# Kernel optimization log

Measured on AMD Instinct MI355X. Metric: run time of the kernel, lower is better.

## Reference

```python
import jax, jax.numpy as jnp
import numpy as np

PC_RANGE = (-54.0, -54.0, -5.0, 54.0, 54.0, 3.0)
VOXEL = (0.075, 0.075, 0.2)
STRIDE = 8
FW = 180  # feature map size along x
FH = 180  # feature map size along y
NUM_CLASS = 2
M = 500   # num_max_objs
MIN_RADIUS = 2
OVERLAP = 0.1
C_IN = 128
HM_C = 2
REG_C = 9
B = 4


def conv2d(x, w, b=None):
    y = jax.lax.conv_general_dilated(x, w, (1, 1), 'SAME',
                                     dimension_numbers=('NCHW', 'OIHW', 'NCHW'))
    return y if b is None else y + b[None, :, None, None]


def bn(x, g, b, m, v, eps=1e-5):
    inv = g / jnp.sqrt(v + eps)
    return x * inv[None, :, None, None] + (b - m * inv)[None, :, None, None]


def gaussian_radius(height, width, min_overlap):
    # centernet_utils.gaussian_radius
    b1 = height + width
    c1 = width * height * (1.0 - min_overlap) / (1.0 + min_overlap)
    r1 = (b1 + jnp.sqrt(jnp.maximum(b1 * b1 - 4.0 * c1, 0.0))) / 2.0
    b2 = 2.0 * (height + width)
    c2 = (1.0 - min_overlap) * width * height
    r2 = (b2 + jnp.sqrt(jnp.maximum(b2 * b2 - 16.0 * c2, 0.0))) / 2.0
    a3 = 4.0 * min_overlap
    b3 = -2.0 * min_overlap * (height + width)
    c3 = (min_overlap - 1.0) * width * height
    r3 = (b3 + jnp.sqrt(jnp.maximum(b3 * b3 - 4.0 * a3 * c3, 0.0))) / (2.0 * a3)
    return jnp.minimum(jnp.minimum(r1, r2), r3)


def assign_targets(gt):
    # gt: (B, M, 8) = [x, y, z, dx, dy, dz, ry, cls]; cls==0 / zero box = padding
    x, y, z = gt[..., 0], gt[..., 1], gt[..., 2]
    dx, dy, dz, ry = gt[..., 3], gt[..., 4], gt[..., 5], gt[..., 6]
    cls = gt[..., 7].astype(jnp.int32)
    coord_x = jnp.clip((x - PC_RANGE[0]) / VOXEL[0] / STRIDE, 0.0, FW - 0.5)
    coord_y = jnp.clip((y - PC_RANGE[1]) / VOXEL[1] / STRIDE, 0.0, FH - 0.5)
    cxi = coord_x.astype(jnp.int32)
    cyi = coord_y.astype(jnp.int32)
    dxp = dx / VOXEL[0] / STRIDE
    dyp = dy / VOXEL[1] / STRIDE
    radius = jnp.maximum(gaussian_radius(dxp, dyp, OVERLAP).astype(jnp.int32), MIN_RADIUS)
    valid = (dxp > 0) & (dyp > 0)
    pos = valid & (cls >= 1)

    # --- dense gaussian splat, max-reduced per class (= draw_gaussian_to_heatmap) ---
    ddx = jnp.arange(FW)[None, None, :] - cxi[..., None]   # (B,M,FW)
    ddy = jnp.arange(FH)[None, None, :] - cyi[..., None]   # (B,M,FH)
    sigma = (2.0 * radius.astype(jnp.float32) + 1.0) / 6.0
    d2 = (ddy[..., :, None] ** 2 + ddx[..., None, :] ** 2).astype(jnp.float32)  # (B,M,FH,FW)
    g = jnp.exp(-d2 / (2.0 * sigma[..., None, None] ** 2))
    win = (jnp.abs(ddy) <= radius[..., None])[..., :, None] & \
          (jnp.abs(ddx) <= radius[..., None])[..., None, :]
    g = jnp.where(win & pos[..., None, None], g, 0.0)
    seg = jnp.where(pos, cls - 1, NUM_CLASS)
    hmv = jax.vmap(lambda gv, sv: jax.ops.segment_max(gv, sv, num_segments=NUM_CLASS + 1))(
        g.reshape(B, M, FH * FW), seg)
    heatmap = jnp.maximum(hmv[:, :NUM_CLASS].reshape(B, NUM_CLASS, FH, FW), 0.0)
    heatmap_mask = (heatmap > 0).astype(gt.dtype)

    # --- inds / mask / ret_boxes (5 slots per object: center + 4 neighbors) ---
    base_ind = cyi * FW + cxi
    w_cond = VOXEL[0] * STRIDE > dy / 4.0   # faithful: uses temp_w = gt[:,4]
    l_cond = VOXEL[1] * STRIDE > dx / 4.0   # faithful: uses temp_l = gt[:,3]
    left = cxi - 1 >= 0
    right = cxi + 1 < FW
    up = cyi - 1 >= 0
    down = cyi + 1 < FH
    m0 = jnp.where(valid, jnp.where(cls >= 1, 1, -1), 0)
    s1 = valid & ~w_cond & left
    s2 = valid & ~w_cond & right
    s3 = valid & ~l_cond & up
    s4 = valid & ~l_cond & down
    mask = jnp.stack([m0,
                      jnp.where(s1, m0, 0), jnp.where(s2, m0, 0),
                      jnp.where(s3, m0, 0), jnp.where(s4, m0, 0)], -1).reshape(B, 5 * M)
    inds = jnp.stack([jnp.where(valid, base_ind, 0),
                      jnp.where(s1, base_ind - 1, 0), jnp.where(s2, base_ind + 1, 0),
                      jnp.where(s3, base_ind - FW, 0), jnp.where(s4, base_ind + FW, 0)],
                     -1).reshape(B, 5 * M).astype(jnp.int32)
    offx = coord_x - cxi.astype(gt.dtype)
    offy = coord_y - cyi.astype(gt.dtype)
    base = jnp.stack([offx, offy, z,
                      jnp.log(jnp.maximum(dx, 1e-8)),
                      jnp.log(jnp.maximum(dy, 1e-8)),
                      jnp.log(jnp.maximum(dz, 1e-8)),
                      jnp.cos(ry), jnp.sin(ry)], -1)          # (B,M,8)
    z5 = jnp.zeros((B, M), gt.dtype)
    dx_adj = jnp.stack([z5, s1.astype(gt.dtype), -s2.astype(gt.dtype), z5, z5], -1)  # (B,M,5)
    dy_adj = jnp.stack([z5, z5, z5, s3.astype(gt.dtype), -s4.astype(gt.dtype)], -1)
    zero5 = jnp.zeros_like(dx_adj)
    delta = jnp.stack([dx_adj, dy_adj, zero5, zero5, zero5, zero5, zero5, zero5], -1)  # (B,M,5,8)
    rb = (base[:, :, None, :] + delta) * valid[:, :, None, None].astype(gt.dtype)
    ret_boxes = rb.reshape(B, 5 * M, 8)
    return heatmap, ret_boxes, inds, mask, heatmap_mask


def setup_inputs():
    key = jax.random.key(0)
    ks = jax.random.split(key, 12)
    x = jax.random.normal(ks[0], (B, C_IN, FH, FW), jnp.float32)
    # realistic gt boxes; last 150 per scene are zero padding
    cxy = jax.random.uniform(ks[1], (B, M, 2), minval=-50.0, maxval=50.0)
    zc = jax.random.uniform(ks[2], (B, M, 1), minval=-2.0, maxval=1.0)
    dims = jax.random.uniform(ks[3], (B, M, 3), minval=0.5, maxval=6.0)
    ry = jax.random.uniform(ks[4], (B, M, 1), minval=-3.14, maxval=3.14)
    cls = jax.random.randint(ks[5], (B, M, 1), 1, NUM_CLASS + 1).astype(jnp.float32)
    vm = (jnp.arange(M) < 350)[None, :, None].astype(jnp.float32)
    gt_boxes = jnp.concatenate([cxy, zc, dims, ry, cls], -1) * vm
    p = lambda k, s, sc: jax.random.normal(k, s, jnp.float32) * sc
    return {
        'x': x, 'gt_boxes': gt_boxes,
        'conv1_w': p(ks[6], (C_IN, C_IN, 3, 3), 0.02),
        'bn1_g': jnp.ones((C_IN,)), 'bn1_b': jnp.zeros((C_IN,)),
        'bn1_m': jnp.zeros((C_IN,)), 'bn1_v': jnp.ones((C_IN,)),
        'conv2_w': p(ks[7], (C_IN, C_IN, 3, 3), 0.02),
        'bn2_g': jnp.ones((C_IN,)), 'bn2_b': jnp.zeros((C_IN,)),
        'bn2_m': jnp.zeros((C_IN,)), 'bn2_v': jnp.ones((C_IN,)),
        'hm_w': p(ks[8], (HM_C, C_IN, 3, 3), 0.02),
        'hm_b': jnp.full((HM_C,), -2.19, jnp.float32),
        'reg_w': p(ks[9], (REG_C, C_IN, 3, 3), 0.001),
        'reg_b': jnp.zeros((REG_C,), jnp.float32),
    }


def reference(x, gt_boxes, conv1_w, bn1_g, bn1_b, bn1_m, bn1_v,
              conv2_w, bn2_g, bn2_b, bn2_m, bn2_v, hm_w, hm_b, reg_w, reg_b):
    f = jax.nn.relu(bn(conv2d(x, conv1_w), bn1_g, bn1_b, bn1_m, bn1_v))
    f = jax.nn.relu(bn(conv2d(f, conv2_w), bn2_g, bn2_b, bn2_m, bn2_v))
    hm = conv2d(f, hm_w, hm_b)      # (B, 2, H, W)
    reg = conv2d(f, reg_w, reg_b)   # (B, 9, H, W)
    heatmap, ret_boxes, inds, mask, heatmap_mask = assign_targets(gt_boxes)
    return hm, reg, heatmap, ret_boxes, inds, mask, heatmap_mask
```

## Files before the change

### kernel.cpp

```cpp
#include <hip/hip_runtime.h>
#include <math.h>

typedef unsigned short u16;
typedef short bf16x8 __attribute__((ext_vector_type(8)));
typedef float f32x4 __attribute__((ext_vector_type(4)));

#define FW_ 180
#define FH_ 180
#define HW_ (FW_*FH_)
#define CIN_ 128
#define BB_ 4
#define MM_ 500
#define PW_ 182
#define PADE ((size_t)BB_*PW_*PW_*CIN_)

#define HM_OFF   0
#define REG_OFF  (BB_*2*HW_)
#define HEAT_OFF (REG_OFF + BB_*9*HW_)
#define RB_OFF   (HEAT_OFF + BB_*2*HW_)
#define IND_OFF  (RB_OFF + BB_*MM_*5*8)
#define MSK_OFF  (IND_OFF + BB_*MM_*5)
#define HMM_OFF  (MSK_OFF + BB_*MM_*5)

__device__ inline u16 f2bf(float f) {
    unsigned u = __float_as_uint(f);
    u += 0x7FFFu + ((u >> 16) & 1u);
    return (u16)(u >> 16);
}

#define GLOAD_LDS16(gsrc, ldst) \
    __builtin_amdgcn_global_load_lds( \
        (const __attribute__((address_space(1))) unsigned*)(gsrc), \
        (__attribute__((address_space(3))) unsigned*)(ldst), 16, 0, 0)

__device__ void obj_work(int ob, int lane, const float* __restrict__ gt,
                         float* __restrict__ out)
{
    int b = ob / MM_, m = ob % MM_;
    const float* gp = gt + (size_t)ob * 8;
    float x = gp[0], y = gp[1], z = gp[2];
    float dx = gp[3], dy = gp[4], dz = gp[5], ry = gp[6];
    int cls = (int)gp[7];

    float coord_x = fminf(fmaxf((x + 54.f) / 0.075f / 8.f, 0.f), 179.5f);
    float coord_y = fminf(fmaxf((y + 54.f) / 0.075f / 8.f, 0.f), 179.5f);
    int cxi = (int)coord_x, cyi = (int)coord_y;
    float dxp = dx / 0.075f / 8.f;
    float dyp = dy / 0.075f / 8.f;

    float hgt = dxp, wid = dyp, mo = 0.1f;
    float b1 = hgt + wid, c1 = wid * hgt * (1.f - mo) / (1.f + mo);
    float r1 = (b1 + sqrtf(fmaxf(b1 * b1 - 4.f * c1, 0.f))) * 0.5f;
    float b2 = 2.f * (hgt + wid), c2 = (1.f - mo) * wid * hgt;
    float r2 = (b2 + sqrtf(fmaxf(b2 * b2 - 16.f * c2, 0.f))) * 0.5f;
    float a3 = 4.f * mo, b3 = -2.f * mo * (hgt + wid), c3 = (mo - 1.f) * wid * hgt;
    float r3 = (b3 + sqrtf(fmaxf(b3 * b3 - 4.f * a3 * c3, 0.f))) / (2.f * a3);
    int radius = max((int)fminf(fminf(r1, r2), r3), 2);

    bool valid = (dxp > 0.f) && (dyp > 0.f);
    bool pos = valid && (cls >= 1);

    if (lane == 0) {
        float m0 = valid ? (cls >= 1 ? 1.f : -1.f) : 0.f;
        bool w_cond = (0.075f * 8.f) > dy / 4.f;
        bool l_cond = (0.075f * 8.f) > dx / 4.f;
        bool s1 = valid && !w_cond && (cxi - 1 >= 0);
        bool s2 = valid && !w_cond && (cxi + 1 < FW_);
        bool s3 = valid && !l_cond && (cyi - 1 >= 0);
        bool s4 = valid && !l_cond && (cyi + 1 < FH_);
        int base_ind = cyi * FW_ + cxi;

        float* indp = out + IND_OFF + (size_t)b * MM_ * 5 + m * 5;
        float* mskp = out + MSK_OFF + (size_t)b * MM_ * 5 + m * 5;
        indp[0] = valid ? (float)base_ind : 0.f;
        indp[1] = s1 ? (float)(base_ind - 1) : 0.f;
        indp[2] = s2 ? (float)(base_ind + 1) : 0.f;
        indp[3] = s3 ? (float)(base_ind - FW_) : 0.f;
        indp[4] = s4 ? (float)(base_ind + FW_) : 0.f;
        mskp[0] = m0;
        mskp[1] = s1 ? m0 : 0.f;
        mskp[2] = s2 ? m0 : 0.f;
        mskp[3] = s3 ? m0 : 0.f;
        mskp[4] = s4 ? m0 : 0.f;

        float offx = coord_x - (float)cxi;
        float offy = coord_y - (float)cyi;
        float bse[8] = { offx, offy, z,
                         logf(fmaxf(dx, 1e-8f)), logf(fmaxf(dy, 1e-8f)),
                         logf(fmaxf(dz, 1e-8f)), cosf(ry), sinf(ry) };
        float vm = valid ? 1.f : 0.f;
        float* rbp = out + RB_OFF + ((size_t)b * MM_ + m) * 5 * 8;
#pragma unroll
        for (int s = 0; s < 5; ++s) {
            float t0 = bse[0], t1 = bse[1];
            if (s == 1) t0 += s1 ? 1.f : 0.f;
            if (s == 2) t0 -= s2 ? 1.f : 0.f;
            if (s == 3) t1 += s3 ? 1.f : 0.f;
            if (s == 4) t1 -= s4 ? 1.f : 0.f;
            rbp[s * 8 + 0] = t0 * vm;
            rbp[s * 8 + 1] = t1 * vm;
#pragma unroll
            for (int k = 2; k < 8; ++k) rbp[s * 8 + k] = bse[k] * vm;
        }
    }

    if (pos) {
        float sigma = (2.f * (float)radius + 1.f) / 6.f;
        float inv2s2 = 1.f / (2.f * sigma * sigma);
        int x0 = max(cxi - radius, 0), x1 = min(cxi + radius, FW_ - 1);
        int y0 = max(cyi - radius, 0), y1 = min(cyi + radius, FH_ - 1);
        int wdt = x1 - x0 + 1, tot = wdt * (y1 - y0 + 1);
        float* hp = out + HEAT_OFF + (size_t)(b * 2 + (cls - 1)) * HW_;
        for (int i = lane; i < tot; i += 64) {
            int yy = y0 + i / wdt, xx = x0 + i % wdt;
            float ddy = (float)(yy - cyi), ddx = (float)(xx - cxi);
            float gvl = expf(-(ddy * ddy + ddx * ddx) * inv2s2);
            atomicMax((int*)(hp + yy * FW_ + xx), __float_as_int(gvl));
        }
    }
}

__global__ __launch_bounds__(256) void k_pre(
    const float* __restrict__ x, u16* __restrict__ xT, u16* __restrict__ ws,
    float* __restrict__ out,
    const float* __restrict__ w1, const float* __restrict__ w2,
    const float* __restrict__ hw, const float* __restrict__ rw,
    u16* __restrict__ wT1, u16* __restrict__ wT2, u16* __restrict__ wTh)
{
    __shared__ unsigned lt32[180 * 65];
    int tid = threadIdx.x;
    if (blockIdx.x < 720) {
        int row = blockIdx.x % 180, b = blockIdx.x / 180;
        const float* inr = x + ((size_t)b * CIN_ * FH_ + row) * FW_;
        for (int i = tid; i < 64 * 45; i += 256) {
            int ci2 = i / 45, c4 = i - 45 * ci2;
            const float* p0 = inr + (size_t)(2 * ci2) * HW_ + c4 * 4;
            float4 a = *(const float4*)p0;
            float4 bq = *(const float4*)(p0 + HW_);
            lt32[(c4 * 4 + 0) * 65 + ci2] = (unsigned)f2bf(a.x) | ((unsigned)f2bf(bq.x) << 16);
            lt32[(c4 * 4 + 1) * 65 + ci2] = (unsigned)f2bf(a.y) | ((unsigned)f2bf(bq.y) << 16);
            lt32[(c4 * 4 + 2) * 65 + ci2] = (unsigned)f2bf(a.z) | ((unsigned)f2bf(bq.z) << 16);
            lt32[(c4 * 4 + 3) * 65 + ci2] = (unsigned)f2bf(a.w) | ((unsigned)f2bf(bq.w) << 16);
        }
        __syncthreads();
        unsigned* dst = (unsigned*)(xT + ((size_t)b * PW_ * PW_ + (size_t)(row + 1) * PW_ + 1) * CIN_);
        for (int idx = tid; idx < 180 * 16; idx += 256) {
            int col = idx >> 4, q = idx & 15;
            uint4 v;
            v.x = lt32[col * 65 + q * 4 + 0];
            v.y = lt32[col * 65 + q * 4 + 1];
            v.z = lt32[col * 65 + q * 4 + 2];
            v.w = lt32[col * 65 + q * 4 + 3];
            *(uint4*)&dst[col * 64 + q * 4] = v;
        }
        return;
    }

    int idx = (blockIdx.x - 720) * 256 + tid;
    if (idx < 12 * 724) {
        int which = idx / 724, cell = idx % 724;
        int buf = which >> 2, b = which & 3;
        int r, c;
        if (cell < 182)      { r = 0;   c = cell; }
        else if (cell < 364) { r = 181; c = cell - 182; }
        else { int s = cell - 364; r = 1 + (s >> 1); c = (s & 1) ? 181 : 0; }
        u16* base = ws + (size_t)buf * PADE + ((size_t)b * PW_ * PW_ + (size_t)r * PW_ + c) * CIN_;
#pragma unroll
        for (int i = 0; i < 16; ++i) ((uint4*)base)[i] = make_uint4(0, 0, 0, 0);
        return;
    }
    idx -= 12 * 724;
    if (idx < BB_ * 2 * HW_) { out[HEAT_OFF + idx] = 0.f; return; }
    idx -= BB_ * 2 * HW_;
    const int NW = 9 * CIN_ * CIN_;
    if (idx < NW) {
        int tap = idx / (CIN_ * CIN_);
        int r = idx % (CIN_ * CIN_);
        int co = r >> 7, ci = r & 127;
        wT1[idx] = f2bf(w1[((size_t)co * CIN_ + ci) * 9 + tap]);
        return;
    }
    idx -= NW;
    if (idx < NW) {
        int tap = idx / (CIN_ * CIN_);
        int r = idx % (CIN_ * CIN_);
        int co = r >> 7, ci = r & 127;
        wT2[idx] = f2bf(w2[((size_t)co * CIN_ + ci) * 9 + tap]);
        return;
    }
    idx -= NW;
    if (idx < 9 * 16 * CIN_) {
        int tap = idx / (16 * CIN_);
        int r = idx % (16 * CIN_);
        int co = r >> 7, ci = r & 127;
        float v = 0.f;
        if (co < 2)       v = hw[((size_t)co * CIN_ + ci) * 9 + tap];
        else if (co < 11) v = rw[((size_t)(co - 2) * CIN_ + ci) * 9 + tap];
        wTh[idx] = f2bf(v);
    }
}

__global__ __launch_bounds__(256, 2) void k_conv_v15(
    const u16* __restrict__ xT, const u16* __restrict__ wT,
    const float* __restrict__ gg, const float* __restrict__ bbn,
    const float* __restrict__ mmn, const float* __restrict__ vvn,
    u16* __restrict__ yT,
    const float* __restrict__ gt, float* __restrict__ outp)
{
    __shared__ u16 lin[1600 * 8];
    __shared__ u16 lwt[3][768 * 8];

    if (blockIdx.x >= 1080) {
        int ob = ((int)blockIdx.x - 1080) * 4 + ((int)threadIdx.x >> 6);
        obj_work(ob, threadIdx.x & 63, gt, outp);
        return;
    }

    int tid  = threadIdx.x;
    int wv   = tid >> 6, lane = tid & 63;
    int lm   = lane & 15, hi = lane >> 4;

    int wg   = blockIdx.x;
    int wgid = (wg & 7) * 135 + (wg >> 3);
    int b    = wgid / 270;
    int rem  = wgid % 270;
    int row  = rem / 6;
    int t6   = rem % 6;
    int csp  = t6 % 3, cog = t6 / 3;
    int C0   = (csp == 2) ? 116 : csp * 64;
    int cob  = cog * 64;
    int R0   = row * 4;
    const u16* xb = xT + (size_t)b * PW_ * PW_ * CIN_;

    f32x4 acc[4][4];
#pragma unroll
    for (int i = 0; i < 4; ++i)
#pragma unroll
        for (int j = 0; j < 4; ++j) acc[i][j] = (f32x4){0.f, 0.f, 0.f, 0.f};

    unsigned soffI[6];
#pragma unroll
    for (int rd = 0; rd < 6; ++rd) {
        int o = rd * 256 + tid;
        int rc = o >> 2;
        int r = rc / 66, c = rc - 66 * r;
        int q = (o & 3) ^ ((c >> 1) & 3);
        soffI[rd] = (unsigned)(((R0 + r) * PW_ + (C0 + c)) * CIN_ + q * 8);
    }
    unsigned soffX = 0;
    if (tid < 64) {
        int o = 1536 + tid;
        int rc = o >> 2;
        int r = rc / 66, c = rc - 66 * r;
        if (o >= 1584) { r = 5; c = 65; }
        int q = (o & 3) ^ ((c >> 1) & 3);
        soffX = (unsigned)(((R0 + r) * PW_ + (C0 + c)) * CIN_ + q * 8);
    }
    const int wco = tid >> 2;
    const int wq  = (tid & 3) ^ ((wco >> 1) & 3);
    const unsigned soffW = (unsigned)((cob + wco) * CIN_ + wq * 8);

    #define STAGE_IN(CH)                                                        \
    {                                                                           \
        _Pragma("unroll")                                                       \
        for (int rd = 0; rd < 6; ++rd)                                          \
            GLOAD_LDS16(xb + soffI[rd] + (CH) * 32,                             \
                        &lin[(size_t)(rd * 256 + wv * 64) * 8]);                \
        if (tid < 64)                                                           \
            GLOAD_LDS16(xb + soffX + (CH) * 32, &lin[(size_t)1536 * 8]);        \
    }
    #define STAGE_W(NCH, NTG)                                                   \
    {                                                                           \
        _Pragma("unroll")                                                       \
        for (int rd = 0; rd < 3; ++rd)                                          \
            GLOAD_LDS16(wT + (size_t)((NTG) * 3 + rd) * CIN_ * CIN_ + soffW + (NCH) * 32, \
                        &lwt[NTG][(size_t)(rd * 256 + wv * 64) * 8]);           \
    }
    #define COMPUTE_TG(TG)                                                      \
    {                                                                           \
        _Pragma("unroll")                                                       \
        for (int t = 0; t < 3; ++t) {                                           \
            bf16x8 av[4];                                                       \
            _Pragma("unroll")                                                   \
            for (int mf = 0; mf < 4; ++mf) {                                    \
                int col = mf * 16 + lm;                                         \
                int unit = t * 256 + col * 4 + (hi ^ ((col >> 1) & 3));         \
                av[mf] = *(const bf16x8*)&lwt[TG][(size_t)unit * 8];            \
            }                                                                   \
            _Pragma("unroll")                                                   \
            for (int nf = 0; nf < 4; ++nf) {                                    \
                int c = wv * 16 + lm + t;                                       \
                int rc = (nf + (TG)) * 66 + c;                                  \
                int unit = rc * 4 + (hi ^ ((c >> 1) & 3));                      \
                bf16x8 bv = *(const bf16x8*)&lin[(size_t)unit * 8];             \
                _Pragma("unroll")                                               \
                for (int mf = 0; mf < 4; ++mf)                                  \
                    acc[mf][nf] = __builtin_amdgcn_mfma_f32_16x16x32_bf16(      \
                        av[mf], bv, acc[mf][nf], 0, 0, 0);                      \
            }                                                                   \
        }                                                                       \
    }

    STAGE_IN(0);
    STAGE_W(0, 0);

#pragma unroll
    for (int ch = 0; ch < 4; ++ch) {
#pragma unroll
        for (int tg = 0; tg < 3; ++tg) {
            if (tg == 0 && ch > 0) {
                __builtin_amdgcn_s_barrier();
                __builtin_amdgcn_sched_barrier(0);
                STAGE_IN(ch);
            }
            const bool last = (ch == 3 && tg == 2);
            if (!last) {
                const int nch = (tg == 2) ? ch + 1 : ch;
                const int ntg = (tg + 1) % 3;
                STAGE_W(nch, ntg);
                asm volatile("s_waitcnt vmcnt(3)" ::: "memory");
            } else {
                asm volatile("s_waitcnt vmcnt(0)" ::: "memory");
            }
            __builtin_amdgcn_s_barrier();
            __builtin_amdgcn_sched_barrier(0);
            COMPUTE_TG(tg);
        }
    }
    #undef STAGE_IN
    #undef STAGE_W
    #undef COMPUTE_TG

#pragma unroll
    for (int mf = 0; mf < 4; ++mf) {
        int co0 = cob + mf * 16 + hi * 4;
        float4 g4 = *(const float4*)(gg + co0);
        float4 b4 = *(const float4*)(bbn + co0);
        float4 m4 = *(const float4*)(mmn + co0);
        float4 v4 = *(const float4*)(vvn + co0);
        float sc0 = g4.x / sqrtf(v4.x + 1e-5f), sh0 = b4.x - m4.x * sc0;
        float sc1 = g4.y / sqrtf(v4.y + 1e-5f), sh1 = b4.y - m4.y * sc1;
        float sc2 = g4.z / sqrtf(v4.z + 1e-5f), sh2 = b4.z - m4.z * sc2;
        float sc3 = g4.w / sqrtf(v4.w + 1e-5f), sh3 = b4.w - m4.w * sc3;
#pragma unroll
        for (int nf = 0; nf < 4; ++nf) {
            f32x4 A = acc[mf][nf];
            float y0 = fmaxf(fmaf(A[0], sc0, sh0), 0.f);
            float y1 = fmaxf(fmaf(A[1], sc1, sh1), 0.f);
            float y2 = fmaxf(fmaf(A[2], sc2, sh2), 0.f);
            float y3 = fmaxf(fmaf(A[3], sc3, sh3), 0.f);
            unsigned p0 = (unsigned)f2bf(y0) | ((unsigned)f2bf(y1) << 16);
            unsigned p1 = (unsigned)f2bf(y2) | ((unsigned)f2bf(y3) << 16);
            u16* op = yT + (size_t)b * PW_ * PW_ * CIN_ +
                      ((size_t)(R0 + nf + 1) * PW_ + (C0 + wv * 16 + lm + 1)) * CIN_ + co0;
            *(uint2*)op = make_uint2(p0, p1);
        }
    }
}

__global__ __launch_bounds__(256) void k_head_v9(
    const u16* __restrict__ f2T, const u16* __restrict__ wTh,
    const float* __restrict__ hb, const float* __restrict__ rb,
    float* __restrict__ out)
{
    __shared__ u16 lin[1600 * 8];
    __shared__ u16 lwt[2304 * 8];

    int tid  = threadIdx.x;
    int wv   = tid >> 6, lane = tid & 63;
    int lm   = lane & 15, hi = lane >> 4;
    int csp  = blockIdx.x;
    int C0   = (csp == 2) ? 116 : csp * 64;
    int R0   = blockIdx.y * 4;
    int b    = blockIdx.z;
    const u16* xb = f2T + (size_t)b * PW_ * PW_ * CIN_;

    f32x4 acc[4];
#pragma unroll
    for (int i = 0; i < 4; ++i) acc[i] = (f32x4){0.f, 0.f, 0.f, 0.f};

#pragma unroll
    for (int rd = 0; rd < 9; ++rd) {
        int o = rd * 256 + tid;
        int tap = o >> 8, rest = o & 255;
        int co = rest >> 4, u8s = rest & 15;
        const u16* src = wTh + (size_t)tap * 16 * CIN_ + co * CIN_ + ((u8s ^ (co & 7)) * 8);
        GLOAD_LDS16(src, &lwt[(size_t)(rd * 256 + wv * 64) * 8]);
    }

#pragma unroll 1
    for (int ch = 0; ch < 4; ++ch) {
        int ci0 = ch * 32;
        __syncthreads();
#pragma unroll
        for (int rd = 0; rd < 6; ++rd) {
            int o = rd * 256 + tid;
            int rc = o >> 2;
            int r = rc / 66, c = rc - 66 * r;
            int q = (o & 3) ^ ((c >> 1) & 3);
            const u16* src = xb + ((size_t)(R0 + r) * PW_ + (C0 + c)) * CIN_ + ci0 + q * 8;
            GLOAD_LDS16(src, &lin[(size_t)(rd * 256 + wv * 64) * 8]);
        }
        if (tid < 64) {
            int o = 1536 + tid;
            int rc = o >> 2;
            int r = rc / 66, c = rc - 66 * r;
            if (o >= 1584) { r = 5; c = 65; }
            int q = (o & 3) ^ ((c >> 1) & 3);
            const u16* src = xb + ((size_t)(R0 + r) * PW_ + (C0 + c)) * CIN_ + ci0 + q * 8;
            GLOAD_LDS16(src, &lin[(size_t)1536 * 8]);
        }
        __syncthreads();

#pragma unroll
        for (int tap = 0; tap < 9; ++tap) {
            const int kr = tap / 3, kc = tap - 3 * (tap / 3);
            int u8 = (ch * 4 + hi) ^ (lm & 7);
            bf16x8 av = *(const bf16x8*)&lwt[(size_t)(tap * 256 + lm * 16 + u8) * 8];
#pragma unroll
            for (int nf = 0; nf < 4; ++nf) {
                int c = wv * 16 + lm + kc;
                int rc = (nf + kr) * 66 + c;
                int unit = rc * 4 + (hi ^ ((c >> 1) & 3));
                bf16x8 bv = *(const bf16x8*)&lin[(size_t)unit * 8];
                acc[nf] = __builtin_amdgcn_mfma_f32_16x16x32_bf16(av, bv, acc[nf], 0, 0, 0);
            }
        }
    }

#pragma unroll
    for (int nf = 0; nf < 4; ++nf) {
        int row = R0 + nf, col = C0 + wv * 16 + lm;
        f32x4 A = acc[nf];
#pragma unroll
        for (int r = 0; r < 4; ++r) {
            int co = hi * 4 + r;
            float v = A[r];
            if (co < 2)
                out[HM_OFF + ((size_t)(b * 2 + co)) * HW_ + (size_t)row * FW_ + col] = v + hb[co];
            else if (co < 11)
                out[REG_OFF + ((size_t)(b * 9 + co - 2)) * HW_ + (size_t)row * FW_ + col] = v + rb[co - 2];
        }
    }

    int blk = (b * 45 + (int)blockIdx.y) * 3 + csp;
    int base = blk * 480;
    for (int i = base + tid; i < base + 480; i += 256) {
        float v = out[HEAT_OFF + i];
        out[HMM_OFF + i] = v > 0.f ? 1.f : 0.f;
    }
}

extern "C" void kernel_launch(void* const* d_in, const int* in_sizes, int n_in,
                              void* d_out, int out_size, void* d_ws, size_t ws_size,
                              hipStream_t stream)
{
    const float* x  = (const float*)d_in[0];
    const float* gt = (const float*)d_in[1];
    const float* w1 = (const float*)d_in[2];
    const float* g1 = (const float*)d_in[3];
    const float* b1 = (const float*)d_in[4];
    const float* m1 = (const float*)d_in[5];
    const float* v1 = (const float*)d_in[6];
    const float* w2 = (const float*)d_in[7];
    const float* g2 = (const float*)d_in[8];
    const float* b2 = (const float*)d_in[9];
    const float* m2 = (const float*)d_in[10];
    const float* v2 = (const float*)d_in[11];
    const float* hw = (const float*)d_in[12];
    const float* hb = (const float*)d_in[13];
    const float* rw = (const float*)d_in[14];
    const float* rb = (const float*)d_in[15];
    float* out = (float*)d_out;

    u16* ws  = (u16*)d_ws;
    u16* xT  = ws;
    u16* f1T = ws + PADE;
    u16* f2T = ws + 2 * PADE;
    u16* wT1 = ws + 3 * PADE;
    u16* wT2 = wT1 + 9 * CIN_ * CIN_;
    u16* wTh = wT2 + 9 * CIN_ * CIN_;

    const int NFLAT = 12 * 724 + BB_ * 2 * HW_ + 2 * 9 * CIN_ * CIN_ + 9 * 16 * CIN_;
    const int NPRE  = 720 + (NFLAT + 255) / 256;
    k_pre<<<NPRE, 256, 0, stream>>>(x, xT, ws, out, w1, w2, hw, rw, wT1, wT2, wTh);

    k_conv_v15<<<1080 + 500, 256, 0, stream>>>(xT,  wT1, g1, b1, m1, v1, f1T, gt, out);
    k_conv_v15<<<1080,       256, 0, stream>>>(f1T, wT2, g2, b2, m2, v2, f2T, gt, out);

    dim3 hg(3, 45, BB_);
    k_head_v9<<<hg, 256, 0, stream>>>(f2T, wTh, hb, rb, out);
}
```

Measured before the change: 137.0 us.

## Prefetch next input chunk into registers to overlap with MFMA compute

The input tile for the 3x3 conv was previously loaded straight into LDS, with a barrier and a load stall at each channel-chunk boundary. It is now loaded into registers one chunk ahead, during the last tap group of the current chunk, and written to LDS after the next barrier. Weight staging is reordered to fit this, with adjusted vmcnt/lgkmcnt waits. The aim is to hide global-load latency behind the matrix-core work, at the cost of extra VGPRs (7 uint4) that could pressure occupancy under launch_bounds(256,2).

After: 176.6 us. +28.9%, slower.

```diff
diff --git a/kernel.cpp b/kernel.cpp
--- a/kernel.cpp
+++ b/kernel.cpp
@@ -200,7 +200,7 @@
     }
 }
 
-__global__ __launch_bounds__(256, 2) void k_conv_v15(
+__global__ __launch_bounds__(256, 2) void k_conv_v16(
     const u16* __restrict__ xT, const u16* __restrict__ wT,
     const float* __restrict__ gg, const float* __restrict__ bbn,
     const float* __restrict__ mmn, const float* __restrict__ vvn,
@@ -247,27 +247,37 @@
         int q = (o & 3) ^ ((c >> 1) & 3);
         soffI[rd] = (unsigned)(((R0 + r) * PW_ + (C0 + c)) * CIN_ + q * 8);
     }
-    unsigned soffX = 0;
-    if (tid < 64) {
-        int o = 1536 + tid;
-        int rc = o >> 2;
+    unsigned soffP = 0;
+    {
+        int uo = 1536 + wv * 16 + (lane & 15);
+        int rc = uo >> 2;
         int r = rc / 66, c = rc - 66 * r;
-        if (o >= 1584) { r = 5; c = 65; }
-        int q = (o & 3) ^ ((c >> 1) & 3);
-        soffX = (unsigned)(((R0 + r) * PW_ + (C0 + c)) * CIN_ + q * 8);
-    }
+        if (uo >= 1584) { r = 5; c = 65; }
+        int q = (uo & 3) ^ ((c >> 1) & 3);
+        soffP = (unsigned)(((R0 + r) * PW_ + (C0 + c)) * CIN_ + q * 8);
+    }
+    const int uP = 1536 + wv * 16 + (lane & 15);
     const int wco = tid >> 2;
     const int wq  = (tid & 3) ^ ((wco >> 1) & 3);
     const unsigned soffW = (unsigned)((cob + wco) * CIN_ + wq * 8);
 
-    #define STAGE_IN(CH)                                                        \
+    uint4 ireg[7];
+
+    #define ILOAD(CH)                                                           \
     {                                                                           \
         _Pragma("unroll")                                                       \
         for (int rd = 0; rd < 6; ++rd)                                          \
-            GLOAD_LDS16(xb + soffI[rd] + (CH) * 32,                             \
-                        &lin[(size_t)(rd * 256 + wv * 64) * 8]);                \
-        if (tid < 64)                                                           \
-            GLOAD_LDS16(xb + soffX + (CH) * 32, &lin[(size_t)1536 * 8]);        \
+            ireg[rd] = *(const uint4*)(xb + soffI[rd] + (CH) * 32);             \
+        if (lane < 16)                                                          \
+            ireg[6] = *(const uint4*)(xb + soffP + (CH) * 32);                  \
+    }
+    #define IWRITE()                                                            \
+    {                                                                           \
+        _Pragma("unroll")                                                       \
+        for (int rd = 0; rd < 6; ++rd)                                          \
+            *(uint4*)&lin[(size_t)(rd * 256 + tid) * 8] = ireg[rd];             \
+        if (lane < 16)                                                          \
+            *(uint4*)&lin[(size_t)uP * 8] = ireg[6];                            \
     }
     #define STAGE_W(NCH, NTG)                                                   \
     {                                                                           \
@@ -301,33 +311,41 @@
         }                                                                       \
     }
 
-    STAGE_IN(0);
+    ILOAD(0);
     STAGE_W(0, 0);
 
 #pragma unroll
     for (int ch = 0; ch < 4; ++ch) {
 #pragma unroll
         for (int tg = 0; tg < 3; ++tg) {
-            if (tg == 0 && ch > 0) {
-                __builtin_amdgcn_s_barrier();
-                __builtin_amdgcn_sched_barrier(0);
-                STAGE_IN(ch);
-            }
-            const bool last = (ch == 3 && tg == 2);
-            if (!last) {
-                const int nch = (tg == 2) ? ch + 1 : ch;
-                const int ntg = (tg + 1) % 3;
-                STAGE_W(nch, ntg);
+            if (tg == 0) {
+                if (ch > 0) {
+                    __builtin_amdgcn_s_barrier();
+                    __builtin_amdgcn_sched_barrier(0);
+                }
+                IWRITE();
+                STAGE_W(ch, 1);
+                asm volatile("s_waitcnt lgkmcnt(0)" ::: "memory");
+                asm volatile("s_waitcnt vmcnt(3)" ::: "memory");
+            } else if (tg == 1) {
+                STAGE_W(ch, 2);
                 asm volatile("s_waitcnt vmcnt(3)" ::: "memory");
             } else {
-                asm volatile("s_waitcnt vmcnt(0)" ::: "memory");
+                if (ch < 3) {
+                    STAGE_W(ch + 1, 0);
+                    ILOAD(ch + 1);
+                    asm volatile("s_waitcnt vmcnt(10)" ::: "memory");
+                } else {
+                    asm volatile("s_waitcnt vmcnt(0)" ::: "memory");
+                }
             }
             __builtin_amdgcn_s_barrier();
             __builtin_amdgcn_sched_barrier(0);
             COMPUTE_TG(tg);
         }
     }
-    #undef STAGE_IN
+    #undef ILOAD
+    #undef IWRITE
     #undef STAGE_W
     #undef COMPUTE_TG
 
@@ -485,8 +503,8 @@
     const int NPRE  = 720 + (NFLAT + 255) / 256;
     k_pre<<<NPRE, 256, 0, stream>>>(x, xT, ws, out, w1, w2, hw, rw, wT1, wT2, wTh);
 
-    k_conv_v15<<<1080 + 500, 256, 0, stream>>>(xT,  wT1, g1, b1, m1, v1, f1T, gt, out);
-    k_conv_v15<<<1080,       256, 0, stream>>>(f1T, wT2, g2, b2, m2, v2, f2T, gt, out);
+    k_conv_v16<<<1080 + 500, 256, 0, stream>>>(xT,  wT1, g1, b1, m1, v1, f1T, gt, out);
+    k_conv_v16<<<1080,       256, 0, stream>>>(f1T, wT2, g2, b2, m2, v2, f2T, gt, out);
 
     dim3 hg(3, 45, BB_);
     k_head_v9<<<hg, 256, 0, stream>>>(f2T, wTh, hb, rb, out);
```
